# Performance work log

Hardware: AMD Instinct MI355X
Metric: run time of the kernel (lower is better)

## Reference

```python
import jax, jax.numpy as jnp
import numpy as np
from jax import lax

KH = KW = 3
K = KH * KW
STRIDE = 1
PAD = 1
DIL = 1
GN_GROUPS = 32
EPS = 1e-5


def setup_inputs() -> dict:
    key = jax.random.key(0)
    k0, k1, k2 = jax.random.split(key, 3)
    B, C, H, W = 8, 256, 64, 64
    O = 256
    x = jax.random.normal(k0, (B, C, H, W), jnp.float32)
    # offset-predicting conv (DeformConv2dPack.conv_offset); small weights keep offsets ~O(1)
    w_off = jax.random.normal(k1, (2 * K, C, KH, KW), jnp.float32) * 0.01
    b_off = jnp.zeros((2 * K,), jnp.float32)
    w_dcn = jax.random.normal(k2, (O, C, KH, KW), jnp.float32) * (1.0 / np.sqrt(C * K))
    gamma = jnp.ones((O,), jnp.float32)
    beta = jnp.zeros((O,), jnp.float32)
    return {"x": x, "w_off": w_off, "b_off": b_off, "w_dcn": w_dcn, "gamma": gamma, "beta": beta}


def _deform_conv(x, w_off, b_off, w_dcn):
    B, C, H, W = x.shape
    O = w_dcn.shape[0]
    # offsets via standard conv: [B, 2K, Ho, Wo]; channel layout (k, (dy, dx))
    offset = lax.conv_general_dilated(
        x, w_off, (STRIDE, STRIDE), [(PAD, PAD), (PAD, PAD)],
        rhs_dilation=(DIL, DIL), dimension_numbers=("NCHW", "OIHW", "NCHW"))
    offset = offset + b_off[None, :, None, None]
    Ho, Wo = offset.shape[2], offset.shape[3]
    off = offset.reshape(B, K, 2, Ho, Wo)
    ky = jnp.repeat(jnp.arange(KH), KW)  # [K]
    kx = jnp.tile(jnp.arange(KW), KH)    # [K]
    base_y = (jnp.arange(Ho) * STRIDE - PAD)[None, :, None] + (ky * DIL)[:, None, None]  # [K,Ho,1]
    base_x = (jnp.arange(Wo) * STRIDE - PAD)[None, None, :] + (kx * DIL)[:, None, None]  # [K,1,Wo]
    py = off[:, :, 0] + base_y[None].astype(off.dtype)  # [B,K,Ho,Wo]
    px = off[:, :, 1] + base_x[None].astype(off.dtype)

    def sample_one(xi, py_i, px_i):  # xi [C,H,W]; py/px [K,Ho,Wo]
        y0 = jnp.floor(py_i)
        x0 = jnp.floor(px_i)
        dy = py_i - y0
        dx = px_i - x0
        y0i = y0.astype(jnp.int32)
        x0i = x0.astype(jnp.int32)

        def gather(yi, xj, w):
            valid = (yi >= 0) & (yi < H) & (xj >= 0) & (xj < W)
            yc = jnp.clip(yi, 0, H - 1)
            xc = jnp.clip(xj, 0, W - 1)
            return xi[:, yc, xc] * (w * valid)[None]  # [C,K,Ho,Wo]

        return (gather(y0i, x0i, (1 - dy) * (1 - dx))
                + gather(y0i, x0i + 1, (1 - dy) * dx)
                + gather(y0i + 1, x0i, dy * (1 - dx))
                + gather(y0i + 1, x0i + 1, dy * dx))

    cols = jax.vmap(sample_one)(x, py, px)  # [B,C,K,Ho,Wo]
    y = jnp.einsum("ock,bckp->bop", w_dcn.reshape(O, C, K),
                   cols.reshape(B, C, K, Ho * Wo))
    return y.reshape(B, O, Ho, Wo)


def _group_norm(y, gamma, beta):
    B, O, Ho, Wo = y.shape
    g = y.reshape(B, GN_GROUPS, O // GN_GROUPS, Ho, Wo)
    mean = g.mean(axis=(2, 3, 4), keepdims=True)
    var = g.var(axis=(2, 3, 4), keepdims=True)
    yn = ((g - mean) * lax.rsqrt(var + EPS)).reshape(B, O, Ho, Wo)
    return yn * gamma[None, :, None, None] + beta[None, :, None, None]


def reference(x, w_off, b_off, w_dcn, gamma, beta):
    y = _deform_conv(x, w_off, b_off, w_dcn)
    y = _group_norm(y, gamma, beta)
    return y * jnp.tanh(jax.nn.softplus(y))  # Mish
```

## Files before the change

kernel.cpp:

```cpp
#include <hip/hip_runtime.h>
#include <hip/hip_bf16.h>
#include <math.h>

typedef __bf16 bf16x8 __attribute__((ext_vector_type(8)));
typedef float f32x4 __attribute__((ext_vector_type(4)));
typedef unsigned int u32;
typedef u32 u32x4 __attribute__((ext_vector_type(4)));
typedef u32 u32x2 __attribute__((ext_vector_type(2)));


__device__ inline u32 pack2bf16(float a, float b) {
  u32 ua = __float_as_uint(a);
  u32 ub = __float_as_uint(b);
  ua += 0x7fffu + ((ua >> 16) & 1u);
  ub += 0x7fffu + ((ub >> 16) & 1u);
  return (ua >> 16) | (ub & 0xffff0000u);
}

__global__ void prep(const float* __restrict__ w_dcn, const float* __restrict__ w_off,
                     unsigned short* __restrict__ wT4, unsigned short* __restrict__ wOffT,
                     float* __restrict__ stats) {
  size_t id = (size_t)blockIdx.x * 256 + threadIdx.x;
  if (id < 589824) {
    int o  = (int)(id / 2304);
    int ck = (int)(id % 2304);
    int k = ck >> 8, c = ck & 255;
    float v = w_dcn[(size_t)(o * 256 + c) * 9 + k];
    u32 uv = __float_as_uint(v);
    uv += 0x7fffu + ((uv >> 16) & 1u);
    int tile = ck >> 6, kk = ck & 63;
    int lin = o * 128 + kk * 2;
    int swz = lin ^ ((o & 7) << 4);
    *(unsigned short*)((char*)wT4 + (size_t)tile * 32768 + swz) = (unsigned short)(uv >> 16);
  } else if (id < 663552) {
    int r = (int)(id - 589824);
    int tile = r >> 11;
    int rr = r & 2047;
    int o = rr >> 6, kk = rr & 63;
    int k = tile >> 2, cc = tile & 3;
    int c = (cc << 6) + kk;
    float v = (o < 18) ? w_off[(size_t)(o * 256 + c) * 9 + k] : 0.f;
    u32 uv = __float_as_uint(v);
    uv += 0x7fffu + ((uv >> 16) & 1u);
    int swz = (o * 128 + kk * 2) ^ ((o & 7) << 4);
    *(unsigned short*)((char*)wOffT + (size_t)tile * 4096 + swz) = (unsigned short)(uv >> 16);
  } else if (id < 664064) {
    stats[id - 663552] = 0.f;
  }
}

__global__ __launch_bounds__(256) void transpose_x(const float* __restrict__ x,
                                                   unsigned short* __restrict__ xT) {
  __shared__ float tl[64][65];
  int bx = blockIdx.x;
  int b = bx >> 8;
  int y = (bx >> 2) & 63;
  int cb = (bx & 3) << 6;
  int t = threadIdx.x;
  int xi = t & 63, cr = t >> 6;
  size_t base = (((size_t)(b * 256 + cb) * 64 + y) << 6);
#pragma unroll
  for (int rep = 0; rep < 16; ++rep) {
    int cl = rep * 4 + cr;
    tl[cl][xi] = x[base + (size_t)cl * 4096 + xi];
  }
  __syncthreads();
  int xw = t & 63, cpair = t >> 6;
#pragma unroll
  for (int r = 0; r < 2; ++r) {
    int cgl = cpair * 2 + r;
    int cg = (cb >> 3) + cgl;
    u32 pk4[4];
#pragma unroll
    for (int i = 0; i < 4; ++i)
      pk4[i] = pack2bf16(tl[cgl * 8 + 2 * i][xw], tl[cgl * 8 + 2 * i + 1][xw]);
    u32x4 v = {pk4[0], pk4[1], pk4[2], pk4[3]};
    *(u32x4*)((char*)xT + (((size_t)b << 21)) + ((size_t)cg << 16) + ((y << 6) + xw) * 16) = v;
  }
}

__global__ __launch_bounds__(256, 2) void conv_offset_mfma(
    const unsigned short* __restrict__ xT, const unsigned short* __restrict__ wOffT,
    float* __restrict__ offs) {
  __shared__ unsigned short A[2][64][64];
  __shared__ unsigned short Bo[2][2048];
  const int bx = blockIdx.x;
  const int lb = ((bx & 7) << 6) + (bx >> 3);
  const int b = lb >> 6;
  const int y = lb & 63;
  const int t = threadIdx.x;
  const int lane = t & 63, wid = t >> 6;
  const char* xTbB = (const char*)xT + ((size_t)b << 21);
  const int p = t >> 2;

  f32x4 acc[2];
  {
    f32x4 z = {0.f, 0.f, 0.f, 0.f};
    acc[0] = z; acc[1] = z;
  }

  u32x4 ra = {0u,0u,0u,0u}, rb = {0u,0u,0u,0u};

  auto issue = [&](int tt, int d) {
    int k = tt >> 2, cc = tt & 3;
    int ky = k / 3, kx = k - ky * 3;
    int ys = y - 1 + ky;
    int xs = p - 1 + kx;
    bool ok = ((unsigned)ys < 64u) && ((unsigned)xs < 64u);
    u32x4 z = {0u,0u,0u,0u};
    ra = z; rb = z;
    if (ok) {
      int cg0 = (cc << 3) + ((t & 3) << 1);
      const char* s0 = xTbB + ((size_t)cg0 << 16) + (((ys << 6) + xs) << 4);
      ra = *(const u32x4*)s0;
      rb = *(const u32x4*)(s0 + 65536);
    }
    __builtin_amdgcn_global_load_lds(
        (const __attribute__((address_space(1))) u32*)((const char*)wOffT + ((size_t)tt << 12) + (wid << 10) + (lane << 4)),
        (__attribute__((address_space(3))) u32*)((char*)&Bo[d][0] + (wid << 10)),
        16, 0, 0);
  };
  auto writeA = [&](int d) {
    char* dst = (char*)&A[d][0][0] + p * 128;
    int b0 = (t & 3) << 5;
    int sw = (p & 7) << 4;
    *(u32x4*)(dst + (b0 ^ sw)) = ra;
    *(u32x4*)(dst + ((b0 + 16) ^ sw)) = rb;
  };

  issue(0, 0);
  writeA(0);
  __syncthreads();

  int cur = 0;
  for (int tt = 0; tt < 36; ++tt) {
    if (tt < 35) issue(tt + 1, cur ^ 1);
#pragma unroll
    for (int s = 0; s < 2; ++s) {
      int row = (wid << 4) + (lane & 15);
      int bir = ((s << 6) + ((lane >> 4) << 4)) ^ ((row & 7) << 4);
      bf16x8 a = *(const bf16x8*)((const char*)&A[cur][0][0] + row * 128 + bir);
#pragma unroll
      for (int j = 0; j < 2; ++j) {
        int o = (j << 4) + (lane & 15);
        int kb = ((s << 6) + ((lane >> 4) << 4)) ^ ((o & 7) << 4);
        bf16x8 bv = *(const bf16x8*)((const char*)&Bo[cur][0] + o * 128 + kb);
        acc[j] = __builtin_amdgcn_mfma_f32_16x16x32_bf16(a, bv, acc[j], 0, 0, 0);
      }
    }
    if (tt < 35) writeA(cur ^ 1);
    __syncthreads();
    cur ^= 1;
  }

#pragma unroll
  for (int j = 0; j < 2; ++j) {
    int o = (j << 4) + (lane & 15);
    if (o < 18) {
#pragma unroll
      for (int r = 0; r < 4; ++r) {
        int pl = (wid << 4) + ((lane >> 4) << 2) + r;
        offs[((size_t)b * 4096 + (y << 6) + pl) * 18 + o] = acc[j][r];
      }
    }
  }
}

union Arena {
  struct {
    unsigned short A[2][128][64];
    unsigned short Bt[2][16384];
  } m;
  unsigned short ytile[256][136];
};

__global__ __launch_bounds__(512, 2) void dcn_main(
    const unsigned short* __restrict__ xT, const float* __restrict__ offs,
    const float* __restrict__ boff, const unsigned short* __restrict__ wT4,
    unsigned short* __restrict__ yb, float* __restrict__ stats) {
  __shared__ Arena ar;
  __shared__ unsigned short poffu[9][128][4];
  __shared__ float pw[9][128][4];

  const int bx = blockIdx.x;
  const int lb = ((bx & 7) << 5) + (bx >> 3);
  const int b = lb >> 5;
  const int pxbase = (lb & 31) << 7;
  const int t = threadIdx.x;
  const int lane = t & 63, wid = t >> 6;
  const bool is_cons = (wid < 4);
  const int obase = (wid & 3) << 6;
  const char* xTbB = (const char*)xT + ((size_t)b << 21);

  const int pwid = wid - 4;
  const int p_my = ((pwid & 1) << 6) + lane;
  const int chalf = pwid >> 1;

  for (int idx = t; idx < 1152; idx += 512) {
    int p = idx / 9, k = idx - p * 9;
    int pxg = pxbase + p;
    int yy = pxg >> 6, xx = pxg & 63;
    const float* op = offs + ((size_t)b * 4096 + pxg) * 18 + k * 2;
    int kyi = k / 3, kxi = k - kyi * 3;
    float py = op[0] + boff[k * 2] + (float)(yy - 1 + kyi);
    float pxf = op[1] + boff[k * 2 + 1] + (float)(xx - 1 + kxi);
    float fy = floorf(py), fx = floorf(pxf);
    float dy = py - fy, dx = pxf - fx;
    int y0 = (int)fy, x0 = (int)fx;
    int y1 = y0 + 1, x1 = x0 + 1;
    float vy0 = ((unsigned)y0 < 64u) ? 1.f : 0.f;
    float vy1 = ((unsigned)y1 < 64u) ? 1.f : 0.f;
    float vx0 = ((unsigned)x0 < 64u) ? 1.f : 0.f;
    float vx1 = ((unsigned)x1 < 64u) ? 1.f : 0.f;
    int y0c = min(max(y0, 0), 63), y1c = min(max(y1, 0), 63);
    int x0c = min(max(x0, 0), 63), x1c = min(max(x1, 0), 63);
    poffu[k][p][0] = (unsigned short)((y0c << 6) + x0c);
    poffu[k][p][1] = (unsigned short)((y0c << 6) + x1c);
    poffu[k][p][2] = (unsigned short)((y1c << 6) + x0c);
    poffu[k][p][3] = (unsigned short)((y1c << 6) + x1c);
    pw[k][p][0] = (1.f - dy) * (1.f - dx) * vy0 * vx0;
    pw[k][p][1] = (1.f - dy) * dx * vy0 * vx1;
    pw[k][p][2] = dy * (1.f - dx) * vy1 * vx0;
    pw[k][p][3] = dy * dx * vy1 * vx1;
  }

  f32x4 acc[8][4];
#pragma unroll
  for (int i = 0; i < 8; ++i)
#pragma unroll
    for (int j = 0; j < 4; ++j) {
      f32x4 z = {0.f, 0.f, 0.f, 0.f};
      acc[i][j] = z;
    }

  __syncthreads();

  auto stage = [&](int nt, int d) {
    int k = nt >> 2, cc = nt & 3;
    int cgb = (cc << 3) + (chalf << 2);
    const char* s0 = xTbB + ((int)poffu[k][p_my][0] << 4);
    const char* s1 = xTbB + ((int)poffu[k][p_my][1] << 4);
    const char* s2 = xTbB + ((int)poffu[k][p_my][2] << 4);
    const char* s3 = xTbB + ((int)poffu[k][p_my][3] << 4);
    u32x4 r0[4], r1[4], r2[4], r3[4];
#pragma unroll
    for (int v = 0; v < 4; ++v) {
      size_t po = ((size_t)(cgb + v) << 16);
      r0[v] = *(const u32x4*)(s0 + po);
      r1[v] = *(const u32x4*)(s1 + po);
      r2[v] = *(const u32x4*)(s2 + po);
      r3[v] = *(const u32x4*)(s3 + po);
    }
    {
      const char* src = (const char*)wT4 + ((size_t)nt << 15) + (pwid << 13);
      char* dstb = (char*)&ar.m.Bt[d][0] + (pwid << 13);
#pragma unroll
      for (int i2 = 0; i2 < 8; ++i2) {
        __builtin_amdgcn_global_load_lds(
            (const __attribute__((address_space(1))) u32*)(src + (i2 << 10) + (lane << 4)),
            (__attribute__((address_space(3))) u32*)(dstb + (i2 << 10)),
            16, 0, 0);
      }
    }
    float w0 = pw[k][p_my][0], w1 = pw[k][p_my][1];
    float w2 = pw[k][p_my][2], w3 = pw[k][p_my][3];
    char* dst = (char*)&ar.m.A[d][0][0] + p_my * 128;
    int sw = (p_my & 7) << 4;
#pragma unroll
    for (int v = 0; v < 4; ++v) {
      u32 o4[4];
#pragma unroll
      for (int e = 0; e < 4; ++e) {
        u32 u0 = r0[v][e], u1 = r1[v][e], u2 = r2[v][e], u3 = r3[v][e];
        float lo = w0 * __uint_as_float(u0 << 16);
        lo = fmaf(w1, __uint_as_float(u1 << 16), lo);
        lo = fmaf(w2, __uint_as_float(u2 << 16), lo);
        lo = fmaf(w3, __uint_as_float(u3 << 16), lo);
        float hi = w0 * __uint_as_float(u0 & 0xffff0000u);
        hi = fmaf(w1, __uint_as_float(u1 & 0xffff0000u), hi);
        hi = fmaf(w2, __uint_as_float(u2 & 0xffff0000u), hi);
        hi = fmaf(w3, __uint_as_float(u3 & 0xffff0000u), hi);
        u32 r;
        asm("v_cvt_pk_bf16_f32 %0, %1, %2" : "=v"(r) : "v"(lo), "v"(hi));
        o4[e] = r;
      }
      u32x4 ov = {o4[0], o4[1], o4[2], o4[3]};
      *(u32x4*)(dst + (((chalf << 6) + (v << 4)) ^ sw)) = ov;
    }
  };

  if (!is_cons) stage(0, 0);
  __syncthreads();

  int cur = 0;
  for (int tt = 0; tt < 36; ++tt) {
    if (is_cons) {
      const char* Abase = (const char*)&ar.m.A[cur][0][0];
      const char* Bbase = (const char*)&ar.m.Bt[cur][0];
      __builtin_amdgcn_s_setprio(1);
#pragma unroll
      for (int s = 0; s < 2; ++s) {
        int kx = (s << 6) + ((lane >> 4) << 4);
        int swl = (lane & 7) << 4;
        bf16x8 a[8], bb[4];
#pragma unroll
        for (int i = 0; i < 8; ++i)
          a[i] = *(const bf16x8*)(Abase + ((i << 4) + (lane & 15)) * 128 + (kx ^ swl));
#pragma unroll
        for (int j = 0; j < 4; ++j)
          bb[j] = *(const bf16x8*)(Bbase + (obase + (j << 4) + (lane & 15)) * 128 + (kx ^ swl));
#pragma unroll
        for (int i = 0; i < 8; ++i)
#pragma unroll
          for (int j = 0; j < 4; ++j)
            acc[i][j] = __builtin_amdgcn_mfma_f32_16x16x32_bf16(a[i], bb[j], acc[i][j], 0, 0, 0);
      }
      __builtin_amdgcn_s_setprio(0);
    } else {
      if (tt < 35) stage(tt + 1, cur ^ 1);
    }
    __syncthreads();
    cur ^= 1;
  }

  if (is_cons) {
#pragma unroll
    for (int j = 0; j < 4; ++j) {
      float s1 = 0.f, s2 = 0.f;
#pragma unroll
      for (int i = 0; i < 8; ++i)
#pragma unroll
        for (int r = 0; r < 4; ++r) {
          float v = acc[i][j][r];
          s1 += v;
          s2 += v * v;
        }
      s1 += __shfl_xor(s1, 1, 64);  s2 += __shfl_xor(s2, 1, 64);
      s1 += __shfl_xor(s1, 2, 64);  s2 += __shfl_xor(s2, 2, 64);
      s1 += __shfl_xor(s1, 4, 64);  s2 += __shfl_xor(s2, 4, 64);
      s1 += __shfl_xor(s1, 16, 64); s2 += __shfl_xor(s2, 16, 64);
      s1 += __shfl_xor(s1, 32, 64); s2 += __shfl_xor(s2, 32, 64);
      if ((lane & 0x37) == 0) {
        int g = (obase + (j << 4) + (lane & 15)) >> 3;
        atomicAdd(&stats[((b << 5) + g) * 2 + 0], s1);
        atomicAdd(&stats[((b << 5) + g) * 2 + 1], s2);
      }
    }
#pragma unroll
    for (int i = 0; i < 8; ++i)
#pragma unroll
      for (int j = 0; j < 4; ++j) {
        int o = obase + (j << 4) + (lane & 15);
        int pxr = (i << 4) + ((lane >> 4) << 2);
        u32 w0, w1;
        asm("v_cvt_pk_bf16_f32 %0, %1, %2" : "=v"(w0) : "v"(acc[i][j][0]), "v"(acc[i][j][1]));
        asm("v_cvt_pk_bf16_f32 %0, %1, %2" : "=v"(w1) : "v"(acc[i][j][2]), "v"(acc[i][j][3]));
        u32x2 wv = {w0, w1};
        *(u32x2*)((char*)ar.ytile + o * 272 + pxr * 2) = wv;
      }
  }
  __syncthreads();
  {
    int o = t >> 1, hf = t & 1;
    const char* srcb = (const char*)ar.ytile + o * 272 + (hf << 7);
    unsigned short* dst = yb + (((size_t)(b * 256 + o)) << 12) + pxbase + (hf << 6);
#pragma unroll
    for (int qq = 0; qq < 8; ++qq)
      *(u32x4*)((char*)dst + (qq << 4)) = *(const u32x4*)(srcb + (qq << 4));
  }
}

__global__ __launch_bounds__(256) void gn_mish(const unsigned short* __restrict__ yb,
                                               const float* __restrict__ stats,
                                               const float* __restrict__ gamma,
                                               const float* __restrict__ beta,
                                               float* __restrict__ out) {
  int v = blockIdx.x * 512 + threadIdx.x;
#pragma unroll
  for (int it = 0; it < 2; ++it, v += 256) {
    int o = (v >> 9) & 255;
    int b = v >> 17;
    float s1 = stats[((b << 5) + (o >> 3)) * 2 + 0];
    float s2 = stats[((b << 5) + (o >> 3)) * 2 + 1];
    float mean = s1 * (1.f / 32768.f);
    float var = s2 * (1.f / 32768.f) - mean * mean;
    float rstd = rsqrtf(var + 1e-5f);
    float ga = gamma[o] * rstd, be = beta[o] - mean * gamma[o] * rstd;
    u32x4 u = *(const u32x4*)(yb + ((size_t)v << 3));
    float res[8];
#pragma unroll
    for (int e = 0; e < 4; ++e) {
      float va = __uint_as_float(u[e] << 16);
      float vb = __uint_as_float(u[e] & 0xffff0000u);
      float v0 = fmaf(va, ga, be);
      float v1 = fmaf(vb, ga, be);
      float e0 = expf(fminf(v0, 15.f));
      float e1 = expf(fminf(v1, 15.f));
      float n0 = e0 * (e0 + 2.f);
      float n1 = e1 * (e1 + 2.f);
      float m0 = v0 * (n0 / (n0 + 2.f));
      float m1 = v1 * (n1 / (n1 + 2.f));
      if (v0 > 15.f) m0 = v0;
      if (v1 > 15.f) m1 = v1;
      res[2 * e] = m0;
      res[2 * e + 1] = m1;
    }
    f32x4 o0 = {res[0], res[1], res[2], res[3]};
    f32x4 o1 = {res[4], res[5], res[6], res[7]};
    float* dst = out + ((size_t)v << 3);
    *(f32x4*)dst = o0;
    *((f32x4*)dst + 1) = o1;
  }
}

extern "C" void kernel_launch(void* const* d_in, const int* in_sizes, int n_in,
                              void* d_out, int out_size, void* d_ws, size_t ws_size,
                              hipStream_t stream) {
  const float* x     = (const float*)d_in[0];
  const float* w_off = (const float*)d_in[1];
  const float* b_off = (const float*)d_in[2];
  const float* w_dcn = (const float*)d_in[3];
  const float* gamma = (const float*)d_in[4];
  const float* beta  = (const float*)d_in[5];
  float* out = (float*)d_out;
  char* ws = (char*)d_ws;
  unsigned short* xT   = (unsigned short*)(ws);
  unsigned short* yb   = (unsigned short*)(ws + 16777216);
  float* offs          = (float*)(ws + 33554432);
  unsigned short* wT4  = (unsigned short*)(ws + 35913728);
  unsigned short* wOffT= (unsigned short*)(ws + 37093376);
  float* stats         = (float*)(ws + 37240832);
  prep<<<dim3(2594), dim3(256), 0, stream>>>(w_dcn, w_off, wT4, wOffT, stats);
  transpose_x<<<dim3(2048), dim3(256), 0, stream>>>(x, xT);
  conv_offset_mfma<<<dim3(512), dim3(256), 0, stream>>>(xT, wOffT, offs);
  dcn_main<<<dim3(256), dim3(512), 0, stream>>>(xT, offs, b_off, wT4, yb, stats);
  gn_mish<<<dim3(2048), dim3(256), 0, stream>>>(yb, stats, gamma, beta, out);
}
```

Measured before the change: 135.3 us.

## Replace producer/consumer warp specialization in dcn_main with 1024-thread uniform pipeline

dcn_main moves from 4 producer plus 4 consumer waves to 16 waves that each gather and interpolate one 8-channel slice per pixel and also run MFMAs on a 32-pixel by 64-channel sub-tile, with register prefetch of the next tile's gathers. The aim is to spread the gather, bilinear interpolation and MFMA work over all waves so gather latency overlaps compute instead of serializing behind four producer waves. The offset conv is also widened to 512 threads covering two output rows per block, halving the block count. The cost is a 1024-thread block with much less MFMA reuse per wave (each A fragment feeds 4 MFMAs), a tighter per-thread register budget, and only one block per CU.

```diff
diff --git a/kernel.cpp b/kernel.cpp
--- a/kernel.cpp
+++ b/kernel.cpp
@@ -79,19 +79,22 @@
   }
 }
 
-__global__ __launch_bounds__(256, 2) void conv_offset_mfma(
+__global__ __launch_bounds__(512, 2) void conv_offset_mfma(
     const unsigned short* __restrict__ xT, const unsigned short* __restrict__ wOffT,
     float* __restrict__ offs) {
-  __shared__ unsigned short A[2][64][64];
+  __shared__ unsigned short A[2][128][64];
   __shared__ unsigned short Bo[2][2048];
   const int bx = blockIdx.x;
-  const int lb = ((bx & 7) << 6) + (bx >> 3);
-  const int b = lb >> 6;
-  const int y = lb & 63;
+  const int lb = ((bx & 7) << 5) + (bx >> 3);
+  const int b = lb >> 5;
+  const int rp = lb & 31;
   const int t = threadIdx.x;
   const int lane = t & 63, wid = t >> 6;
   const char* xTbB = (const char*)xT + ((size_t)b << 21);
   const int p = t >> 2;
+  const int row = (rp << 1) + (p >> 6);
+  const int xx = p & 63;
+  const int cpl = (t & 3) << 1;
 
   f32x4 acc[2];
   {
@@ -104,21 +107,21 @@
   auto issue = [&](int tt, int d) {
     int k = tt >> 2, cc = tt & 3;
     int ky = k / 3, kx = k - ky * 3;
-    int ys = y - 1 + ky;
-    int xs = p - 1 + kx;
+    int ys = row - 1 + ky;
+    int xs = xx - 1 + kx;
     bool ok = ((unsigned)ys < 64u) && ((unsigned)xs < 64u);
     u32x4 z = {0u,0u,0u,0u};
     ra = z; rb = z;
     if (ok) {
-      int cg0 = (cc << 3) + ((t & 3) << 1);
-      const char* s0 = xTbB + ((size_t)cg0 << 16) + (((ys << 6) + xs) << 4);
+      const char* s0 = xTbB + ((size_t)(cc * 8 + cpl) << 16) + (((ys << 6) + xs) << 4);
       ra = *(const u32x4*)s0;
       rb = *(const u32x4*)(s0 + 65536);
     }
-    __builtin_amdgcn_global_load_lds(
-        (const __attribute__((address_space(1))) u32*)((const char*)wOffT + ((size_t)tt << 12) + (wid << 10) + (lane << 4)),
-        (__attribute__((address_space(3))) u32*)((char*)&Bo[d][0] + (wid << 10)),
-        16, 0, 0);
+    if (wid < 4)
+      __builtin_amdgcn_global_load_lds(
+          (const __attribute__((address_space(1))) u32*)((const char*)wOffT + ((size_t)tt << 12) + (wid << 10) + (lane << 4)),
+          (__attribute__((address_space(3))) u32*)((char*)&Bo[d][0] + (wid << 10)),
+          16, 0, 0);
   };
   auto writeA = [&](int d) {
     char* dst = (char*)&A[d][0][0] + p * 128;
@@ -137,14 +140,13 @@
     if (tt < 35) issue(tt + 1, cur ^ 1);
 #pragma unroll
     for (int s = 0; s < 2; ++s) {
-      int row = (wid << 4) + (lane & 15);
-      int bir = ((s << 6) + ((lane >> 4) << 4)) ^ ((row & 7) << 4);
-      bf16x8 a = *(const bf16x8*)((const char*)&A[cur][0][0] + row * 128 + bir);
+      int r16 = (wid << 4) + (lane & 15);
+      int kx = (s << 6) + ((lane >> 4) << 4);
+      bf16x8 a = *(const bf16x8*)((const char*)&A[cur][0][0] + r16 * 128 + (kx ^ ((r16 & 7) << 4)));
 #pragma unroll
       for (int j = 0; j < 2; ++j) {
         int o = (j << 4) + (lane & 15);
-        int kb = ((s << 6) + ((lane >> 4) << 4)) ^ ((o & 7) << 4);
-        bf16x8 bv = *(const bf16x8*)((const char*)&Bo[cur][0] + o * 128 + kb);
+        bf16x8 bv = *(const bf16x8*)((const char*)&Bo[cur][0] + o * 128 + (kx ^ ((o & 7) << 4)));
         acc[j] = __builtin_amdgcn_mfma_f32_16x16x32_bf16(a, bv, acc[j], 0, 0, 0);
       }
     }
@@ -160,7 +162,7 @@
 #pragma unroll
       for (int r = 0; r < 4; ++r) {
         int pl = (wid << 4) + ((lane >> 4) << 2) + r;
-        offs[((size_t)b * 4096 + (y << 6) + pl) * 18 + o] = acc[j][r];
+        offs[((size_t)b * 4096 + (rp << 7) + pl) * 18 + o] = acc[j][r];
       }
     }
   }
@@ -174,7 +176,7 @@
   unsigned short ytile[256][136];
 };
 
-__global__ __launch_bounds__(512, 2) void dcn_main(
+__global__ __launch_bounds__(1024) void dcn_main(
     const unsigned short* __restrict__ xT, const float* __restrict__ offs,
     const float* __restrict__ boff, const unsigned short* __restrict__ wT4,
     unsigned short* __restrict__ yb, float* __restrict__ stats) {
@@ -188,15 +190,14 @@
   const int pxbase = (lb & 31) << 7;
   const int t = threadIdx.x;
   const int lane = t & 63, wid = t >> 6;
-  const bool is_cons = (wid < 4);
+  const char* xTbB = (const char*)xT + ((size_t)b << 21);
+
+  const int p_my = (wid << 3) + (lane & 7);
+  const int g_my = lane >> 3;
+  const int pxb = (wid >> 2) << 5;
   const int obase = (wid & 3) << 6;
-  const char* xTbB = (const char*)xT + ((size_t)b << 21);
-
-  const int pwid = wid - 4;
-  const int p_my = ((pwid & 1) << 6) + lane;
-  const int chalf = pwid >> 1;
-
-  for (int idx = t; idx < 1152; idx += 512) {
+
+  for (int idx = t; idx < 1152; idx += 1024) {
     int p = idx / 9, k = idx - p * 9;
     int pxg = pxbase + p;
     int yy = pxg >> 6, xx = pxg & 63;
@@ -224,9 +225,9 @@
     pw[k][p][3] = dy * dx * vy1 * vx1;
   }
 
-  f32x4 acc[8][4];
-#pragma unroll
-  for (int i = 0; i < 8; ++i)
+  f32x4 acc[2][4];
+#pragma unroll
+  for (int i = 0; i < 2; ++i)
 #pragma unroll
     for (int j = 0; j < 4; ++j) {
       f32x4 z = {0.f, 0.f, 0.f, 0.f};
@@ -235,137 +236,134 @@
 
   __syncthreads();
 
-  auto stage = [&](int nt, int d) {
-    int k = nt >> 2, cc = nt & 3;
-    int cgb = (cc << 3) + (chalf << 2);
-    const char* s0 = xTbB + ((int)poffu[k][p_my][0] << 4);
-    const char* s1 = xTbB + ((int)poffu[k][p_my][1] << 4);
-    const char* s2 = xTbB + ((int)poffu[k][p_my][2] << 4);
-    const char* s3 = xTbB + ((int)poffu[k][p_my][3] << 4);
-    u32x4 r0[4], r1[4], r2[4], r3[4];
-#pragma unroll
-    for (int v = 0; v < 4; ++v) {
-      size_t po = ((size_t)(cgb + v) << 16);
-      r0[v] = *(const u32x4*)(s0 + po);
-      r1[v] = *(const u32x4*)(s1 + po);
-      r2[v] = *(const u32x4*)(s2 + po);
-      r3[v] = *(const u32x4*)(s3 + po);
-    }
-    {
-      const char* src = (const char*)wT4 + ((size_t)nt << 15) + (pwid << 13);
-      char* dstb = (char*)&ar.m.Bt[d][0] + (pwid << 13);
-#pragma unroll
-      for (int i2 = 0; i2 < 8; ++i2) {
-        __builtin_amdgcn_global_load_lds(
-            (const __attribute__((address_space(1))) u32*)(src + (i2 << 10) + (lane << 4)),
-            (__attribute__((address_space(3))) u32*)(dstb + (i2 << 10)),
-            16, 0, 0);
-      }
-    }
-    float w0 = pw[k][p_my][0], w1 = pw[k][p_my][1];
-    float w2 = pw[k][p_my][2], w3 = pw[k][p_my][3];
-    char* dst = (char*)&ar.m.A[d][0][0] + p_my * 128;
-    int sw = (p_my & 7) << 4;
-#pragma unroll
-    for (int v = 0; v < 4; ++v) {
-      u32 o4[4];
-#pragma unroll
-      for (int e = 0; e < 4; ++e) {
-        u32 u0 = r0[v][e], u1 = r1[v][e], u2 = r2[v][e], u3 = r3[v][e];
-        float lo = w0 * __uint_as_float(u0 << 16);
-        lo = fmaf(w1, __uint_as_float(u1 << 16), lo);
-        lo = fmaf(w2, __uint_as_float(u2 << 16), lo);
-        lo = fmaf(w3, __uint_as_float(u3 << 16), lo);
-        float hi = w0 * __uint_as_float(u0 & 0xffff0000u);
-        hi = fmaf(w1, __uint_as_float(u1 & 0xffff0000u), hi);
-        hi = fmaf(w2, __uint_as_float(u2 & 0xffff0000u), hi);
-        hi = fmaf(w3, __uint_as_float(u3 & 0xffff0000u), hi);
-        u32 r;
-        asm("v_cvt_pk_bf16_f32 %0, %1, %2" : "=v"(r) : "v"(lo), "v"(hi));
-        o4[e] = r;
-      }
-      u32x4 ov = {o4[0], o4[1], o4[2], o4[3]};
-      *(u32x4*)(dst + (((chalf << 6) + (v << 4)) ^ sw)) = ov;
-    }
+  u32x4 r0, r1, r2, r3;
+  float w0, w1, w2, w3;
+
+  auto issueA = [&](int tt) {
+    int k = tt >> 2, cc = tt & 3;
+    size_t po = (size_t)(cc * 8 + g_my) << 16;
+    const char* base = xTbB + po;
+    w0 = pw[k][p_my][0]; w1 = pw[k][p_my][1];
+    w2 = pw[k][p_my][2]; w3 = pw[k][p_my][3];
+    r0 = *(const u32x4*)(base + ((int)poffu[k][p_my][0] << 4));
+    r1 = *(const u32x4*)(base + ((int)poffu[k][p_my][1] << 4));
+    r2 = *(const u32x4*)(base + ((int)poffu[k][p_my][2] << 4));
+    r3 = *(const u32x4*)(base + ((int)poffu[k][p_my][3] << 4));
   };
-
-  if (!is_cons) stage(0, 0);
+  auto issueB = [&](int tt, int d) {
+    const char* src = (const char*)wT4 + ((size_t)tt << 15) + (wid << 11);
+    char* dstb = (char*)&ar.m.Bt[d][0] + (wid << 11);
+#pragma unroll
+    for (int i2 = 0; i2 < 2; ++i2) {
+      __builtin_amdgcn_global_load_lds(
+          (const __attribute__((address_space(1))) u32*)(src + (i2 << 10) + (lane << 4)),
+          (__attribute__((address_space(3))) u32*)(dstb + (i2 << 10)),
+          16, 0, 0);
+    }
+  };
+  auto packA = [&](int d) {
+    u32 o4[4];
+#pragma unroll
+    for (int e = 0; e < 4; ++e) {
+      u32 u0 = r0[e], u1 = r1[e], u2 = r2[e], u3 = r3[e];
+      float lo = w0 * __uint_as_float(u0 << 16);
+      lo = fmaf(w1, __uint_as_float(u1 << 16), lo);
+      lo = fmaf(w2, __uint_as_float(u2 << 16), lo);
+      lo = fmaf(w3, __uint_as_float(u3 << 16), lo);
+      float hi = w0 * __uint_as_float(u0 & 0xffff0000u);
+      hi = fmaf(w1, __uint_as_float(u1 & 0xffff0000u), hi);
+      hi = fmaf(w2, __uint_as_float(u2 & 0xffff0000u), hi);
+      hi = fmaf(w3, __uint_as_float(u3 & 0xffff0000u), hi);
+      u32 r;
+      asm("v_cvt_pk_bf16_f32 %0, %1, %2" : "=v"(r) : "v"(lo), "v"(hi));
+      o4[e] = r;
+    }
+    u32x4 ov = {o4[0], o4[1], o4[2], o4[3]};
+    *(u32x4*)((char*)&ar.m.A[d][0][0] + p_my * 128 + ((g_my << 4) ^ ((p_my & 7) << 4))) = ov;
+  };
+
+  issueA(0);
+  issueB(0, 0);
+  packA(0);
   __syncthreads();
 
   int cur = 0;
   for (int tt = 0; tt < 36; ++tt) {
-    if (is_cons) {
+    if (tt < 35) { issueA(tt + 1); issueB(tt + 1, cur ^ 1); }
+    {
       const char* Abase = (const char*)&ar.m.A[cur][0][0];
       const char* Bbase = (const char*)&ar.m.Bt[cur][0];
       __builtin_amdgcn_s_setprio(1);
 #pragma unroll
       for (int s = 0; s < 2; ++s) {
         int kx = (s << 6) + ((lane >> 4) << 4);
-        int swl = (lane & 7) << 4;
-        bf16x8 a[8], bb[4];
-#pragma unroll
-        for (int i = 0; i < 8; ++i)
-          a[i] = *(const bf16x8*)(Abase + ((i << 4) + (lane & 15)) * 128 + (kx ^ swl));
-#pragma unroll
-        for (int j = 0; j < 4; ++j)
-          bb[j] = *(const bf16x8*)(Bbase + (obase + (j << 4) + (lane & 15)) * 128 + (kx ^ swl));
-#pragma unroll
-        for (int i = 0; i < 8; ++i)
+        bf16x8 a[2], bb[4];
+#pragma unroll
+        for (int i = 0; i < 2; ++i) {
+          int r16 = pxb + (i << 4) + (lane & 15);
+          a[i] = *(const bf16x8*)(Abase + r16 * 128 + (kx ^ ((r16 & 7) << 4)));
+        }
+#pragma unroll
+        for (int j = 0; j < 4; ++j) {
+          int o = obase + (j << 4) + (lane & 15);
+          bb[j] = *(const bf16x8*)(Bbase + o * 128 + (kx ^ ((o & 7) << 4)));
+        }
+#pragma unroll
+        for (int i = 0; i < 2; ++i)
 #pragma unroll
           for (int j = 0; j < 4; ++j)
             acc[i][j] = __builtin_amdgcn_mfma_f32_16x16x32_bf16(a[i], bb[j], acc[i][j], 0, 0, 0);
       }
       __builtin_amdgcn_s_setprio(0);
-    } else {
-      if (tt < 35) stage(tt + 1, cur ^ 1);
-    }
+    }
+    __builtin_amdgcn_sched_barrier(0);
+    if (tt < 35) packA(cur ^ 1);
     __syncthreads();
     cur ^= 1;
   }
 
-  if (is_cons) {
+#pragma unroll
+  for (int j = 0; j < 4; ++j) {
+    float s1 = 0.f, s2 = 0.f;
+#pragma unroll
+    for (int i = 0; i < 2; ++i)
+#pragma unroll
+      for (int r = 0; r < 4; ++r) {
+        float v = acc[i][j][r];
+        s1 += v;
+        s2 += v * v;
+      }
+    s1 += __shfl_xor(s1, 1, 64);  s2 += __shfl_xor(s2, 1, 64);
+    s1 += __shfl_xor(s1, 2, 64);  s2 += __shfl_xor(s2, 2, 64);
+    s1 += __shfl_xor(s1, 4, 64);  s2 += __shfl_xor(s2, 4, 64);
+    s1 += __shfl_xor(s1, 16, 64); s2 += __shfl_xor(s2, 16, 64);
+    s1 += __shfl_xor(s1, 32, 64); s2 += __shfl_xor(s2, 32, 64);
+    if ((lane & 0x37) == 0) {
+      int g = (obase + (j << 4) + (lane & 15)) >> 3;
+      atomicAdd(&stats[((b << 5) + g) * 2 + 0], s1);
+      atomicAdd(&stats[((b << 5) + g) * 2 + 1], s2);
+    }
+  }
+
+#pragma unroll
+  for (int i = 0; i < 2; ++i)
 #pragma unroll
     for (int j = 0; j < 4; ++j) {
-      float s1 = 0.f, s2 = 0.f;
-#pragma unroll
-      for (int i = 0; i < 8; ++i)
-#pragma unroll
-        for (int r = 0; r < 4; ++r) {
-          float v = acc[i][j][r];
-          s1 += v;
-          s2 += v * v;
-        }
-      s1 += __shfl_xor(s1, 1, 64);  s2 += __shfl_xor(s2, 1, 64);
-      s1 += __shfl_xor(s1, 2, 64);  s2 += __shfl_xor(s2, 2, 64);
-      s1 += __shfl_xor(s1, 4, 64);  s2 += __shfl_xor(s2, 4, 64);
-      s1 += __shfl_xor(s1, 16, 64); s2 += __shfl_xor(s2, 16, 64);
-      s1 += __shfl_xor(s1, 32, 64); s2 += __shfl_xor(s2, 32, 64);
-      if ((lane & 0x37) == 0) {
-        int g = (obase + (j << 4) + (lane & 15)) >> 3;
-        atomicAdd(&stats[((b << 5) + g) * 2 + 0], s1);
-        atomicAdd(&stats[((b << 5) + g) * 2 + 1], s2);
-      }
-    }
-#pragma unroll
-    for (int i = 0; i < 8; ++i)
-#pragma unroll
-      for (int j = 0; j < 4; ++j) {
-        int o = obase + (j << 4) + (lane & 15);
-        int pxr = (i << 4) + ((lane >> 4) << 2);
-        u32 w0, w1;
-        asm("v_cvt_pk_bf16_f32 %0, %1, %2" : "=v"(w0) : "v"(acc[i][j][0]), "v"(acc[i][j][1]));
-        asm("v_cvt_pk_bf16_f32 %0, %1, %2" : "=v"(w1) : "v"(acc[i][j][2]), "v"(acc[i][j][3]));
-        u32x2 wv = {w0, w1};
-        *(u32x2*)((char*)ar.ytile + o * 272 + pxr * 2) = wv;
-      }
-  }
+      int o = obase + (j << 4) + (lane & 15);
+      int pxr = pxb + (i << 4) + ((lane >> 4) << 2);
+      u32 wv0, wv1;
+      asm("v_cvt_pk_bf16_f32 %0, %1, %2" : "=v"(wv0) : "v"(acc[i][j][0]), "v"(acc[i][j][1]));
+      asm("v_cvt_pk_bf16_f32 %0, %1, %2" : "=v"(wv1) : "v"(acc[i][j][2]), "v"(acc[i][j][3]));
+      u32x2 wv = {wv0, wv1};
+      *(u32x2*)((char*)ar.ytile + o * 272 + pxr * 2) = wv;
+    }
   __syncthreads();
   {
-    int o = t >> 1, hf = t & 1;
-    const char* srcb = (const char*)ar.ytile + o * 272 + (hf << 7);
-    unsigned short* dst = yb + (((size_t)(b * 256 + o)) << 12) + pxbase + (hf << 6);
-#pragma unroll
-    for (int qq = 0; qq < 8; ++qq)
+    int o = t >> 2, part = t & 3;
+    const char* srcb = (const char*)ar.ytile + o * 272 + (part << 6);
+    unsigned short* dst = yb + (((size_t)(b * 256 + o)) << 12) + pxbase + (part << 5);
+#pragma unroll
+    for (int qq = 0; qq < 4; ++qq)
       *(u32x4*)((char*)dst + (qq << 4)) = *(const u32x4*)(srcb + (qq << 4));
   }
 }
@@ -432,7 +430,7 @@
   float* stats         = (float*)(ws + 37240832);
   prep<<<dim3(2594), dim3(256), 0, stream>>>(w_dcn, w_off, wT4, wOffT, stats);
   transpose_x<<<dim3(2048), dim3(256), 0, stream>>>(x, xT);
-  conv_offset_mfma<<<dim3(512), dim3(256), 0, stream>>>(xT, wOffT, offs);
-  dcn_main<<<dim3(256), dim3(512), 0, stream>>>(xT, offs, b_off, wT4, yb, stats);
+  conv_offset_mfma<<<dim3(256), dim3(512), 0, stream>>>(xT, wOffT, offs);
+  dcn_main<<<dim3(256), dim3(1024), 0, stream>>>(xT, offs, b_off, wT4, yb, stats);
   gn_mish<<<dim3(2048), dim3(256), 0, stream>>>(yb, stats, gamma, beta, out);
 }
```

After: 147.5 us. 9.0% more time.
